# Kernel optimization log

Hardware: AMD Instinct MI355X
Metric: run time of the kernel (lower is better)

The kernel has to match this reference:

```python
import jax, jax.numpy as jnp
import numpy as np

N_NODES = 100_000
DEG = 16
N_EDGES = N_NODES * DEG
NODE_F = 128
EDGE_F = 16
HID = 64
B = 64
K = DEG


def setup_inputs() -> dict:
    key = jax.random.key(0)
    ks = jax.random.split(key, 12)
    # node i's outgoing edges are at ids i + k*N_NODES for k in [0, DEG)
    src = jnp.arange(N_EDGES, dtype=jnp.int32) % N_NODES
    dst = jax.random.randint(ks[0], (N_EDGES,), 0, N_NODES, dtype=jnp.int32)
    edge_index = jnp.stack([src, dst])
    current_nodes = jax.random.randint(ks[1], (B,), 0, N_NODES, dtype=jnp.int32)
    # reachable neighbors = destinations of the current node's real edges
    neighbor_nodes = dst[current_nodes[:, None] + jnp.arange(K, dtype=jnp.int32)[None, :] * N_NODES]
    x = jax.random.normal(ks[2], (N_NODES, NODE_F), jnp.float32)
    edge_attr = jax.random.normal(ks[3], (N_EDGES, EDGE_F), jnp.float32)
    return dict(
        x=x,
        edge_attr=edge_attr,
        conv1_W=jax.random.normal(ks[4], (NODE_F, HID), jnp.float32) * (NODE_F ** -0.5),
        conv1_b=jnp.zeros((HID,), jnp.float32),
        conv2_W=jax.random.normal(ks[5], (HID, HID), jnp.float32) * (HID ** -0.5),
        conv2_b=jnp.zeros((HID,), jnp.float32),
        mlp_W1=jax.random.normal(ks[6], (2 * HID + EDGE_F, 2 * HID), jnp.float32) * ((2 * HID + EDGE_F) ** -0.5),
        mlp_b1=jnp.zeros((2 * HID,), jnp.float32),
        mlp_W2=jax.random.normal(ks[7], (2 * HID, 1), jnp.float32) * ((2 * HID) ** -0.5),
        mlp_b2=jnp.zeros((1,), jnp.float32),
        edge_index=edge_index,
        current_nodes=current_nodes,
        neighbor_nodes=neighbor_nodes,
    )


def gcn_conv(x, edge_index, W, b):
    """PyG GCNConv: symmetric norm with self-loops, then linear + bias."""
    n = x.shape[0]
    loop = jnp.arange(n, dtype=edge_index.dtype)
    src = jnp.concatenate([edge_index[0], loop])  # messages flow src -> dst
    dst = jnp.concatenate([edge_index[1], loop])
    xw = x @ W                                    # [N, H]
    deg = jnp.zeros((n,), xw.dtype).at[dst].add(1.0)
    dinv = jnp.where(deg > 0, jax.lax.rsqrt(deg), 0.0)
    msg = (dinv[src] * dinv[dst])[:, None] * xw[src]      # [E+N, H]
    return jax.ops.segment_sum(msg, dst, num_segments=n) + b


def reference(x, edge_attr, conv1_W, conv1_b, conv2_W, conv2_b,
              mlp_W1, mlp_b1, mlp_W2, mlp_b2,
              edge_index, current_nodes, neighbor_nodes):
    n = x.shape[0]
    h = jax.nn.relu(gcn_conv(x, edge_index, conv1_W, conv1_b))
    h = jax.nn.relu(gcn_conv(h, edge_index, conv2_W, conv2_b))

    # First edge id matching each (current, neighbor) pair, replacing the
    # original O(E)-per-neighbor boolean-mask loop with a sorted-key lookup.
    keys = edge_index[0].astype(jnp.int64) * n + edge_index[1].astype(jnp.int64)
    order = jnp.argsort(keys, stable=True)        # stable -> leftmost == first edge id
    skeys = keys[order]
    query = current_nodes[:, None].astype(jnp.int64) * n + neighbor_nodes.astype(jnp.int64)
    pos = jnp.clip(jnp.searchsorted(skeys, query), 0, skeys.shape[0] - 1)
    valid = skeys[pos] == query                   # [B, K]
    eid = order[pos]
    ea = edge_attr[eid]                           # [B, K, F]

    b_, k_ = neighbor_nodes.shape
    h_cur = jnp.broadcast_to(h[current_nodes][:, None, :], (b_, k_, h.shape[1]))
    h_nbr = h[neighbor_nodes]
    m = jnp.concatenate([h_cur, h_nbr, ea], axis=-1)  # [B, K, 2H+F]
    q = (jax.nn.relu(m @ mlp_W1 + mlp_b1) @ mlp_W2 + mlp_b2)[..., 0]
    q = jnp.where(valid, q, 0.0)
    return q, valid
```

## Files before the change

### kernel.cpp

```cpp
#include <hip/hip_runtime.h>

#define N_NODES 100000
#define DEG 16
#define N_EDGES (N_NODES * DEG)
#define NODE_F 128
#define EDGE_F 16
#define HID 64
#define NQ 1024
#define NCHUNK (N_EDGES / 256)
#define XTILES ((N_NODES + 63) / 64)
#define NHIST 2048
#define BCAP 56
#define NDINV ((N_NODES + 255) / 256)
#define MAGIC 0x13579BDF

__device__ __forceinline__ int xcc_id() {
  int x;
  asm("s_getreg_b32 %0, hwreg(HW_REG_XCC_ID)" : "=s"(x));
  return x & 7;
}

__global__ void k_query_zero(const int* __restrict__ dst, const int* __restrict__ cur,
                             const int* __restrict__ nbr, int* __restrict__ n1,
                             int* __restrict__ n2, int* __restrict__ wcur,
                             int* __restrict__ eid_sel, float* __restrict__ out_valid,
                             int* __restrict__ degp) {
  if (blockIdx.x >= 4) {
    int4* d4 = (int4*)degp;
    const int n4 = 8 * N_NODES / 4;
    int i = (blockIdx.x - 4) * 256 + threadIdx.x;
    const int stride = (gridDim.x - 4) * 256;
    for (; i < n4; i += stride) d4[i] = make_int4(0, 0, 0, 0);
    return;
  }
  int i = blockIdx.x * 256 + threadIdx.x;
  if (i >= NQ) return;
  int b = i >> 4;
  int c = cur[b];
  int nb = nbr[i];
  int sel = -1;
  #pragma unroll
  for (int j = 0; j < DEG; ++j) {
    int e = c + j * N_NODES;
    if (sel < 0 && dst[e] == nb) sel = e;
  }
  eid_sel[i] = sel;
  out_valid[i] = (sel >= 0) ? 1.0f : 0.0f;
  n2[c] = MAGIC; n2[nb] = MAGIC;
  n1[c] = MAGIC; n1[nb] = MAGIC;
  wcur[c] = 0;   wcur[nb] = 0;
}

__global__ __launch_bounds__(256) void k_fusedA(
    const float* __restrict__ x, const float* __restrict__ Wg,
    float* __restrict__ xw, const int* __restrict__ dst,
    const int* __restrict__ n2, int* __restrict__ n1, int* __restrict__ wcur,
    int* __restrict__ degp) {
  __shared__ float xs[64 * 128];
  const int t = threadIdx.x;

  if (blockIdx.x < NHIST) {
    int* __restrict__ dp = degp + (size_t)xcc_id() * N_NODES;
    const int stride = NHIST * 256;
    for (int e = blockIdx.x * 256 + t; e < N_EDGES; e += stride) {
      int d = dst[e];
      __hip_atomic_fetch_add(&dp[d], 1, __ATOMIC_RELAXED,
                             __HIP_MEMORY_SCOPE_WORKGROUP);
      if (n2[d] == MAGIC) {
        int s = e % N_NODES;
        n1[s] = MAGIC;
        wcur[s] = 0;
      }
    }
    return;
  }

  const int lane = t & 63;
  const int w = __builtin_amdgcn_readfirstlane(t >> 6);
  const long base = (long)(blockIdx.x - NHIST) * 64;

  const float4* __restrict__ xv = (const float4*)x;
  #pragma unroll
  for (int p = 0; p < 8; ++p) {
    int f4 = p * 256 + t;
    int r = f4 >> 5;
    int c4 = f4 & 31;
    long gr = base + r;
    float4 v = (gr < N_NODES) ? xv[gr * 32 + c4]
                              : make_float4(0.f, 0.f, 0.f, 0.f);
    int rs = r & 31;
    float* xr = xs + r * 128;
    xr[((c4 << 2) + 0) ^ rs] = v.x;
    xr[((c4 << 2) + 1) ^ rs] = v.y;
    xr[((c4 << 2) + 2) ^ rs] = v.z;
    xr[((c4 << 2) + 3) ^ rs] = v.w;
  }
  __syncthreads();

  float acc[16];
  #pragma unroll
  for (int j = 0; j < 16; ++j) acc[j] = 0.f;
  const int ls = lane & 31;
  const float* __restrict__ xrow = xs + lane * 128;
  const float4* __restrict__ wp = (const float4*)(Wg + w * 16);
  #pragma unroll 4
  for (int k = 0; k < NODE_F; ++k) {
    float xk = xrow[k ^ ls];
    float4 w0 = wp[k * 16 + 0];
    float4 w1 = wp[k * 16 + 1];
    float4 w2 = wp[k * 16 + 2];
    float4 w3 = wp[k * 16 + 3];
    acc[ 0] = fmaf(xk, w0.x, acc[ 0]); acc[ 1] = fmaf(xk, w0.y, acc[ 1]);
    acc[ 2] = fmaf(xk, w0.z, acc[ 2]); acc[ 3] = fmaf(xk, w0.w, acc[ 3]);
    acc[ 4] = fmaf(xk, w1.x, acc[ 4]); acc[ 5] = fmaf(xk, w1.y, acc[ 5]);
    acc[ 6] = fmaf(xk, w1.z, acc[ 6]); acc[ 7] = fmaf(xk, w1.w, acc[ 7]);
    acc[ 8] = fmaf(xk, w2.x, acc[ 8]); acc[ 9] = fmaf(xk, w2.y, acc[ 9]);
    acc[10] = fmaf(xk, w2.z, acc[10]); acc[11] = fmaf(xk, w2.w, acc[11]);
    acc[12] = fmaf(xk, w3.x, acc[12]); acc[13] = fmaf(xk, w3.y, acc[13]);
    acc[14] = fmaf(xk, w3.z, acc[14]); acc[15] = fmaf(xk, w3.w, acc[15]);
  }
  long gr = base + lane;
  if (gr < N_NODES) {
    float4* __restrict__ op = (float4*)(xw + gr * HID + w * 16);
    op[0] = make_float4(acc[0], acc[1], acc[2], acc[3]);
    op[1] = make_float4(acc[4], acc[5], acc[6], acc[7]);
    op[2] = make_float4(acc[8], acc[9], acc[10], acc[11]);
    op[3] = make_float4(acc[12], acc[13], acc[14], acc[15]);
  }
}

__global__ void k_bucket_dinv(const int* __restrict__ dst, const int* __restrict__ n1,
                              int* __restrict__ wcur, int* __restrict__ bucket,
                              const int* __restrict__ degp, float* __restrict__ dinv) {
  if (blockIdx.x < NDINV) {
    int v = blockIdx.x * 256 + threadIdx.x;
    if (v < N_NODES) {
      int s = 1;
      #pragma unroll
      for (int p = 0; p < 8; ++p) s += degp[(size_t)p * N_NODES + v];
      dinv[v] = rsqrtf((float)s);
    }
    return;
  }
  int e = (blockIdx.x - NDINV) * 256 + threadIdx.x;
  int d = dst[e];
  if (n1[d] != MAGIC) return;
  int pos = atomicAdd(&wcur[d], 1);
  if (pos >= 0 && pos < BCAP)
    bucket[(size_t)d * BCAP + pos] = e % N_NODES;
}

__global__ __launch_bounds__(256) void k_gather_xw2(
    const int* __restrict__ bucket, const int* __restrict__ wcur,
    const int* __restrict__ n1, const float* __restrict__ dinv,
    const float* __restrict__ xw, const float* __restrict__ bias,
    const float* __restrict__ W2g, float* __restrict__ xw2) {
  const int t = threadIdx.x;
  const int lane = t & 63;
  const int v = blockIdx.x * 4 + (t >> 6);
  if (v >= N_NODES) return;
  if (n1[v] != MAGIC) return;
  int n = wcur[v];
  if (n > BCAP) n = BCAP;
  if (n < 0) n = 0;
  int   s_l = (lane < n) ? bucket[(size_t)v * BCAP + lane] : 0;
  float w_l = (lane < n) ? dinv[s_l] : 0.f;
  float acc = 0.f;
  int j = 0;
  for (; j + 3 < n; j += 4) {
    int s0 = __shfl(s_l, j);
    int s1 = __shfl(s_l, j + 1);
    int s2 = __shfl(s_l, j + 2);
    int s3 = __shfl(s_l, j + 3);
    float a0 = xw[(size_t)s0 * HID + lane];
    float a1 = xw[(size_t)s1 * HID + lane];
    float a2 = xw[(size_t)s2 * HID + lane];
    float a3 = xw[(size_t)s3 * HID + lane];
    acc = fmaf(__shfl(w_l, j), a0, acc);
    acc = fmaf(__shfl(w_l, j + 1), a1, acc);
    acc = fmaf(__shfl(w_l, j + 2), a2, acc);
    acc = fmaf(__shfl(w_l, j + 3), a3, acc);
  }
  for (; j < n; ++j)
    acc = fmaf(__shfl(w_l, j), xw[(size_t)__shfl(s_l, j) * HID + lane], acc);
  float dv = dinv[v];
  acc = fmaf(dv, xw[(size_t)v * HID + lane], acc);
  float h = fmaxf(fmaf(dv, acc, bias[lane]), 0.f);
  float a2s = 0.f;
  #pragma unroll
  for (int f = 0; f < HID; ++f)
    a2s = fmaf(__shfl(h, f), W2g[f * HID + lane], a2s);
  xw2[(size_t)v * HID + lane] = a2s;
}

__global__ __launch_bounds__(256) void k_gather(
    const int* __restrict__ bucket, const int* __restrict__ wcur,
    const int* __restrict__ flag, const float* __restrict__ dinv,
    const float* __restrict__ xw, const float* __restrict__ bias,
    float* __restrict__ hout) {
  const int t = threadIdx.x;
  const int lane = t & 63;
  const int v = blockIdx.x * 4 + (t >> 6);
  if (v >= N_NODES) return;
  if (flag[v] != MAGIC) return;
  int n = wcur[v];
  if (n > BCAP) n = BCAP;
  if (n < 0) n = 0;
  int   s_l = (lane < n) ? bucket[(size_t)v * BCAP + lane] : 0;
  float w_l = (lane < n) ? dinv[s_l] : 0.f;
  float acc = 0.f;
  int j = 0;
  for (; j + 3 < n; j += 4) {
    int s0 = __shfl(s_l, j);
    int s1 = __shfl(s_l, j + 1);
    int s2 = __shfl(s_l, j + 2);
    int s3 = __shfl(s_l, j + 3);
    float a0 = xw[(size_t)s0 * HID + lane];
    float a1 = xw[(size_t)s1 * HID + lane];
    float a2 = xw[(size_t)s2 * HID + lane];
    float a3 = xw[(size_t)s3 * HID + lane];
    acc = fmaf(__shfl(w_l, j), a0, acc);
    acc = fmaf(__shfl(w_l, j + 1), a1, acc);
    acc = fmaf(__shfl(w_l, j + 2), a2, acc);
    acc = fmaf(__shfl(w_l, j + 3), a3, acc);
  }
  for (; j < n; ++j)
    acc = fmaf(__shfl(w_l, j), xw[(size_t)__shfl(s_l, j) * HID + lane], acc);
  float dv = dinv[v];
  acc = fmaf(dv, xw[(size_t)v * HID + lane], acc);
  hout[(size_t)v * HID + lane] = fmaxf(fmaf(dv, acc, bias[lane]), 0.f);
}

__global__ void k_mlp(const float* __restrict__ h2, const float* __restrict__ ea,
                      const float* __restrict__ W1, const float* __restrict__ b1,
                      const float* __restrict__ W2, const float* __restrict__ b2,
                      const int* __restrict__ cur, const int* __restrict__ nbr,
                      const int* __restrict__ eid_sel, float* __restrict__ out) {
  __shared__ float m[2 * HID + EDGE_F];
  __shared__ float red[128];
  const int q = blockIdx.x;
  const int t = threadIdx.x;
  const int eid = eid_sel[q];
  if (eid < 0) {
    if (t == 0) out[q] = 0.0f;
    return;
  }
  const int b = q >> 4;
  const int c = cur[b];
  const int nb = nbr[q];
  if (t < HID)    m[t] = h2[(size_t)c * HID + t];
  else            m[t] = h2[(size_t)nb * HID + (t - HID)];
  if (t < EDGE_F) m[2 * HID + t] = ea[(size_t)eid * EDGE_F + t];
  __syncthreads();
  float h = b1[t];
  #pragma unroll
  for (int j = 0; j < 2 * HID + EDGE_F; ++j) h = fmaf(m[j], W1[j * 128 + t], h);
  h = fmaxf(h, 0.f) * W2[t];
  red[t] = h;
  __syncthreads();
  if (t < 64) {
    float v = red[t] + red[t + 64];
    #pragma unroll
    for (int o = 32; o > 0; o >>= 1) v += __shfl_down(v, o);
    if (t == 0) out[q] = v + b2[0];
  }
}

extern "C" void kernel_launch(void* const* d_in, const int* in_sizes, int n_in,
                              void* d_out, int out_size, void* d_ws, size_t ws_size,
                              hipStream_t stream) {
  const float* x    = (const float*)d_in[0];
  const float* ea   = (const float*)d_in[1];
  const float* c1W  = (const float*)d_in[2];
  const float* c1b  = (const float*)d_in[3];
  const float* c2W  = (const float*)d_in[4];
  const float* c2b  = (const float*)d_in[5];
  const float* mW1  = (const float*)d_in[6];
  const float* mb1  = (const float*)d_in[7];
  const float* mW2  = (const float*)d_in[8];
  const float* mb2  = (const float*)d_in[9];
  const int*   eidx = (const int*)d_in[10];
  const int*   cur  = (const int*)d_in[11];
  const int*   nbr  = (const int*)d_in[12];
  const int* edst = eidx + N_EDGES;
  float* out = (float*)d_out;

  char* p = (char*)d_ws;
  auto alloc = [&](size_t bytes) -> void* {
    void* r = (void*)p;
    p += (bytes + 255) & ~(size_t)255;
    return r;
  };
  int*   degp    = (int*)alloc((size_t)8 * N_NODES * 4);
  float* dinv    = (float*)alloc((size_t)N_NODES * 4);
  int*   n1      = (int*)alloc((size_t)N_NODES * 4);
  int*   n2      = (int*)alloc((size_t)N_NODES * 4);
  int*   wcur    = (int*)alloc((size_t)N_NODES * 4);
  int*   eid_sel = (int*)alloc((size_t)NQ * 4);
  int*   bucket  = (int*)alloc((size_t)N_NODES * BCAP * 4);
  float* xw1     = (float*)alloc((size_t)N_NODES * HID * 4);
  float* xw2     = (float*)alloc((size_t)N_NODES * HID * 4);
  float* h2      = xw1;

  k_query_zero<<<260, 256, 0, stream>>>(edst, cur, nbr, n1, n2, wcur, eid_sel,
                                        out + NQ, degp);
  k_fusedA<<<NHIST + XTILES, 256, 0, stream>>>(x, c1W, xw1, edst, n2, n1, wcur,
                                               degp);
  k_bucket_dinv<<<NDINV + NCHUNK, 256, 0, stream>>>(edst, n1, wcur, bucket, degp,
                                                    dinv);
  k_gather_xw2<<<(N_NODES + 3) / 4, 256, 0, stream>>>(bucket, wcur, n1, dinv, xw1,
                                                      c1b, c2W, xw2);
  k_gather<<<(N_NODES + 3) / 4, 256, 0, stream>>>(bucket, wcur, n2, dinv, xw2,
                                                  c2b, h2);
  k_mlp<<<NQ, 128, 0, stream>>>(h2, ea, mW1, mb1, mW2, mb2, cur, nbr, eid_sel, out);
}
```

Measured before the change: 354.9 us.

## Fuse degree histogram into bucket fill and derive dinv from bucket counts

Drops the per-XCC degree histogram and the separate bucket/dinv kernel. The edge pass in the fused kernel now does a device-scope atomicAdd on wcur for every edge and writes the bucket entry directly, so wcur doubles as the in-degree and dinv is computed on the fly with rsqrt. The gather kernels now use float4 loads in which four 16-lane groups each handle one neighbor and are combined with xor shuffles. In exchange, all 1.6M edges do global device-scope atomics and scattered bucket writes instead of only edges into flagged nodes, and one kernel launch is removed.

```diff
diff --git a/kernel.cpp b/kernel.cpp
--- a/kernel.cpp
+++ b/kernel.cpp
@@ -7,27 +7,18 @@
 #define EDGE_F 16
 #define HID 64
 #define NQ 1024
-#define NCHUNK (N_EDGES / 256)
 #define XTILES ((N_NODES + 63) / 64)
-#define NHIST 2048
+#define NB 3072
 #define BCAP 56
-#define NDINV ((N_NODES + 255) / 256)
 #define MAGIC 0x13579BDF
-
-__device__ __forceinline__ int xcc_id() {
-  int x;
-  asm("s_getreg_b32 %0, hwreg(HW_REG_XCC_ID)" : "=s"(x));
-  return x & 7;
-}
 
 __global__ void k_query_zero(const int* __restrict__ dst, const int* __restrict__ cur,
                              const int* __restrict__ nbr, int* __restrict__ n1,
                              int* __restrict__ n2, int* __restrict__ wcur,
-                             int* __restrict__ eid_sel, float* __restrict__ out_valid,
-                             int* __restrict__ degp) {
+                             int* __restrict__ eid_sel, float* __restrict__ out_valid) {
   if (blockIdx.x >= 4) {
-    int4* d4 = (int4*)degp;
-    const int n4 = 8 * N_NODES / 4;
+    int4* d4 = (int4*)wcur;
+    const int n4 = N_NODES / 4;
     int i = (blockIdx.x - 4) * 256 + threadIdx.x;
     const int stride = (gridDim.x - 4) * 256;
     for (; i < n4; i += stride) d4[i] = make_int4(0, 0, 0, 0);
@@ -48,36 +39,31 @@
   out_valid[i] = (sel >= 0) ? 1.0f : 0.0f;
   n2[c] = MAGIC; n2[nb] = MAGIC;
   n1[c] = MAGIC; n1[nb] = MAGIC;
-  wcur[c] = 0;   wcur[nb] = 0;
-}
-
-__global__ __launch_bounds__(256) void k_fusedA(
+}
+
+__global__ __launch_bounds__(256) void k_fusedB(
     const float* __restrict__ x, const float* __restrict__ Wg,
     float* __restrict__ xw, const int* __restrict__ dst,
-    const int* __restrict__ n2, int* __restrict__ n1, int* __restrict__ wcur,
-    int* __restrict__ degp) {
+    const int* __restrict__ n2, int* __restrict__ n1,
+    int* __restrict__ wcur, int* __restrict__ bucket) {
   __shared__ float xs[64 * 128];
   const int t = threadIdx.x;
 
-  if (blockIdx.x < NHIST) {
-    int* __restrict__ dp = degp + (size_t)xcc_id() * N_NODES;
-    const int stride = NHIST * 256;
+  if (blockIdx.x < NB) {
+    const int stride = NB * 256;
     for (int e = blockIdx.x * 256 + t; e < N_EDGES; e += stride) {
       int d = dst[e];
-      __hip_atomic_fetch_add(&dp[d], 1, __ATOMIC_RELAXED,
-                             __HIP_MEMORY_SCOPE_WORKGROUP);
-      if (n2[d] == MAGIC) {
-        int s = e % N_NODES;
-        n1[s] = MAGIC;
-        wcur[s] = 0;
-      }
+      int pos = atomicAdd(&wcur[d], 1);
+      int s = e % N_NODES;
+      if (pos < BCAP) bucket[(size_t)d * BCAP + pos] = s;
+      if (n2[d] == MAGIC) n1[s] = MAGIC;
     }
     return;
   }
 
   const int lane = t & 63;
   const int w = __builtin_amdgcn_readfirstlane(t >> 6);
-  const long base = (long)(blockIdx.x - NHIST) * 64;
+  const long base = (long)(blockIdx.x - NB) * 64;
 
   const float4* __restrict__ xv = (const float4*)x;
   #pragma unroll
@@ -129,106 +115,78 @@
   }
 }
 
-__global__ void k_bucket_dinv(const int* __restrict__ dst, const int* __restrict__ n1,
-                              int* __restrict__ wcur, int* __restrict__ bucket,
-                              const int* __restrict__ degp, float* __restrict__ dinv) {
-  if (blockIdx.x < NDINV) {
-    int v = blockIdx.x * 256 + threadIdx.x;
-    if (v < N_NODES) {
-      int s = 1;
-      #pragma unroll
-      for (int p = 0; p < 8; ++p) s += degp[(size_t)p * N_NODES + v];
-      dinv[v] = rsqrtf((float)s);
-    }
-    return;
-  }
-  int e = (blockIdx.x - NDINV) * 256 + threadIdx.x;
-  int d = dst[e];
-  if (n1[d] != MAGIC) return;
-  int pos = atomicAdd(&wcur[d], 1);
-  if (pos >= 0 && pos < BCAP)
-    bucket[(size_t)d * BCAP + pos] = e % N_NODES;
+__device__ __forceinline__ bool gather_core(
+    int v, const int* __restrict__ bucket, const int* __restrict__ wcur,
+    const int* __restrict__ flag, const float* __restrict__ xw,
+    const float* __restrict__ bias, int lane, float4& h4) {
+  if (flag[v] != MAGIC) return false;
+  int nraw = wcur[v];
+  float dv = rsqrtf((float)(nraw + 1));
+  int n = nraw < BCAP ? nraw : BCAP;
+  const int g = lane >> 4, q = lane & 15;
+  int   s_l = (lane < n) ? bucket[(size_t)v * BCAP + lane] : 0;
+  float w_l = (lane < n) ? rsqrtf((float)(wcur[s_l] + 1)) : 0.f;
+  float4 acc = make_float4(0.f, 0.f, 0.f, 0.f);
+  for (int j = 0; j < n; j += 4) {
+    int jj = j + g;
+    int   s = __shfl(s_l, jj);
+    float w = __shfl(w_l, jj);
+    float4 a = ((const float4*)(xw + (size_t)s * HID))[q];
+    acc.x = fmaf(w, a.x, acc.x);
+    acc.y = fmaf(w, a.y, acc.y);
+    acc.z = fmaf(w, a.z, acc.z);
+    acc.w = fmaf(w, a.w, acc.w);
+  }
+  acc.x += __shfl_xor(acc.x, 16); acc.y += __shfl_xor(acc.y, 16);
+  acc.z += __shfl_xor(acc.z, 16); acc.w += __shfl_xor(acc.w, 16);
+  acc.x += __shfl_xor(acc.x, 32); acc.y += __shfl_xor(acc.y, 32);
+  acc.z += __shfl_xor(acc.z, 32); acc.w += __shfl_xor(acc.w, 32);
+  float4 self = ((const float4*)(xw + (size_t)v * HID))[q];
+  float4 b4 = ((const float4*)bias)[q];
+  h4.x = fmaxf(fmaf(dv, fmaf(dv, self.x, acc.x), b4.x), 0.f);
+  h4.y = fmaxf(fmaf(dv, fmaf(dv, self.y, acc.y), b4.y), 0.f);
+  h4.z = fmaxf(fmaf(dv, fmaf(dv, self.z, acc.z), b4.z), 0.f);
+  h4.w = fmaxf(fmaf(dv, fmaf(dv, self.w, acc.w), b4.w), 0.f);
+  return true;
 }
 
 __global__ __launch_bounds__(256) void k_gather_xw2(
     const int* __restrict__ bucket, const int* __restrict__ wcur,
-    const int* __restrict__ n1, const float* __restrict__ dinv,
-    const float* __restrict__ xw, const float* __restrict__ bias,
-    const float* __restrict__ W2g, float* __restrict__ xw2) {
+    const int* __restrict__ n1, const float* __restrict__ xw,
+    const float* __restrict__ bias, const float* __restrict__ W2g,
+    float* __restrict__ xw2) {
   const int t = threadIdx.x;
   const int lane = t & 63;
   const int v = blockIdx.x * 4 + (t >> 6);
   if (v >= N_NODES) return;
-  if (n1[v] != MAGIC) return;
-  int n = wcur[v];
-  if (n > BCAP) n = BCAP;
-  if (n < 0) n = 0;
-  int   s_l = (lane < n) ? bucket[(size_t)v * BCAP + lane] : 0;
-  float w_l = (lane < n) ? dinv[s_l] : 0.f;
-  float acc = 0.f;
-  int j = 0;
-  for (; j + 3 < n; j += 4) {
-    int s0 = __shfl(s_l, j);
-    int s1 = __shfl(s_l, j + 1);
-    int s2 = __shfl(s_l, j + 2);
-    int s3 = __shfl(s_l, j + 3);
-    float a0 = xw[(size_t)s0 * HID + lane];
-    float a1 = xw[(size_t)s1 * HID + lane];
-    float a2 = xw[(size_t)s2 * HID + lane];
-    float a3 = xw[(size_t)s3 * HID + lane];
-    acc = fmaf(__shfl(w_l, j), a0, acc);
-    acc = fmaf(__shfl(w_l, j + 1), a1, acc);
-    acc = fmaf(__shfl(w_l, j + 2), a2, acc);
-    acc = fmaf(__shfl(w_l, j + 3), a3, acc);
-  }
-  for (; j < n; ++j)
-    acc = fmaf(__shfl(w_l, j), xw[(size_t)__shfl(s_l, j) * HID + lane], acc);
-  float dv = dinv[v];
-  acc = fmaf(dv, xw[(size_t)v * HID + lane], acc);
-  float h = fmaxf(fmaf(dv, acc, bias[lane]), 0.f);
-  float a2s = 0.f;
-  #pragma unroll
-  for (int f = 0; f < HID; ++f)
-    a2s = fmaf(__shfl(h, f), W2g[f * HID + lane], a2s);
-  xw2[(size_t)v * HID + lane] = a2s;
+  float4 h4;
+  if (!gather_core(v, bucket, wcur, n1, xw, bias, lane, h4)) return;
+  float a2 = 0.f;
+  #pragma unroll
+  for (int qq = 0; qq < 16; ++qq) {
+    float hx = __shfl(h4.x, qq);
+    float hy = __shfl(h4.y, qq);
+    float hz = __shfl(h4.z, qq);
+    float hw = __shfl(h4.w, qq);
+    a2 = fmaf(hx, W2g[(4 * qq + 0) * HID + lane], a2);
+    a2 = fmaf(hy, W2g[(4 * qq + 1) * HID + lane], a2);
+    a2 = fmaf(hz, W2g[(4 * qq + 2) * HID + lane], a2);
+    a2 = fmaf(hw, W2g[(4 * qq + 3) * HID + lane], a2);
+  }
+  xw2[(size_t)v * HID + lane] = a2;
 }
 
 __global__ __launch_bounds__(256) void k_gather(
     const int* __restrict__ bucket, const int* __restrict__ wcur,
-    const int* __restrict__ flag, const float* __restrict__ dinv,
-    const float* __restrict__ xw, const float* __restrict__ bias,
-    float* __restrict__ hout) {
+    const int* __restrict__ flag, const float* __restrict__ xw,
+    const float* __restrict__ bias, float* __restrict__ hout) {
   const int t = threadIdx.x;
   const int lane = t & 63;
   const int v = blockIdx.x * 4 + (t >> 6);
   if (v >= N_NODES) return;
-  if (flag[v] != MAGIC) return;
-  int n = wcur[v];
-  if (n > BCAP) n = BCAP;
-  if (n < 0) n = 0;
-  int   s_l = (lane < n) ? bucket[(size_t)v * BCAP + lane] : 0;
-  float w_l = (lane < n) ? dinv[s_l] : 0.f;
-  float acc = 0.f;
-  int j = 0;
-  for (; j + 3 < n; j += 4) {
-    int s0 = __shfl(s_l, j);
-    int s1 = __shfl(s_l, j + 1);
-    int s2 = __shfl(s_l, j + 2);
-    int s3 = __shfl(s_l, j + 3);
-    float a0 = xw[(size_t)s0 * HID + lane];
-    float a1 = xw[(size_t)s1 * HID + lane];
-    float a2 = xw[(size_t)s2 * HID + lane];
-    float a3 = xw[(size_t)s3 * HID + lane];
-    acc = fmaf(__shfl(w_l, j), a0, acc);
-    acc = fmaf(__shfl(w_l, j + 1), a1, acc);
-    acc = fmaf(__shfl(w_l, j + 2), a2, acc);
-    acc = fmaf(__shfl(w_l, j + 3), a3, acc);
-  }
-  for (; j < n; ++j)
-    acc = fmaf(__shfl(w_l, j), xw[(size_t)__shfl(s_l, j) * HID + lane], acc);
-  float dv = dinv[v];
-  acc = fmaf(dv, xw[(size_t)v * HID + lane], acc);
-  hout[(size_t)v * HID + lane] = fmaxf(fmaf(dv, acc, bias[lane]), 0.f);
+  float4 h4;
+  if (!gather_core(v, bucket, wcur, flag, xw, bias, lane, h4)) return;
+  if (lane < 16) ((float4*)(hout + (size_t)v * HID))[lane] = h4;
 }
 
 __global__ void k_mlp(const float* __restrict__ h2, const float* __restrict__ ea,
@@ -291,8 +249,6 @@
     p += (bytes + 255) & ~(size_t)255;
     return r;
   };
-  int*   degp    = (int*)alloc((size_t)8 * N_NODES * 4);
-  float* dinv    = (float*)alloc((size_t)N_NODES * 4);
   int*   n1      = (int*)alloc((size_t)N_NODES * 4);
   int*   n2      = (int*)alloc((size_t)N_NODES * 4);
   int*   wcur    = (int*)alloc((size_t)N_NODES * 4);
@@ -302,15 +258,12 @@
   float* xw2     = (float*)alloc((size_t)N_NODES * HID * 4);
   float* h2      = xw1;
 
-  k_query_zero<<<260, 256, 0, stream>>>(edst, cur, nbr, n1, n2, wcur, eid_sel,
-                                        out + NQ, degp);
-  k_fusedA<<<NHIST + XTILES, 256, 0, stream>>>(x, c1W, xw1, edst, n2, n1, wcur,
-                                               degp);
-  k_bucket_dinv<<<NDINV + NCHUNK, 256, 0, stream>>>(edst, n1, wcur, bucket, degp,
-                                                    dinv);
-  k_gather_xw2<<<(N_NODES + 3) / 4, 256, 0, stream>>>(bucket, wcur, n1, dinv, xw1,
-                                                      c1b, c2W, xw2);
-  k_gather<<<(N_NODES + 3) / 4, 256, 0, stream>>>(bucket, wcur, n2, dinv, xw2,
-                                                  c2b, h2);
+  k_query_zero<<<104, 256, 0, stream>>>(edst, cur, nbr, n1, n2, wcur, eid_sel,
+                                        out + NQ);
+  k_fusedB<<<NB + XTILES, 256, 0, stream>>>(x, c1W, xw1, edst, n2, n1, wcur,
+                                            bucket);
+  k_gather_xw2<<<N_NODES / 4, 256, 0, stream>>>(bucket, wcur, n1, xw1, c1b,
+                                                c2W, xw2);
+  k_gather<<<N_NODES / 4, 256, 0, stream>>>(bucket, wcur, n2, xw2, c2b, h2);
   k_mlp<<<NQ, 128, 0, stream>>>(h2, ea, mW1, mb1, mW2, mb2, cur, nbr, eid_sel, out);
 }
```

Result: slower. 377.7 us (+6.4%).
